# Kernel tuning notes

Hardware: AMD Instinct MI355X
Metric: run time of the kernel (lower is better)

## Reference

```python
import jax, jax.numpy as jnp
import numpy as np

C, P, G = 80, 30000, 800       # classes, preds/class, gts/class
IOU_THR = 0.5
IMG = 1024.0                   # synthetic image size
BATCH = 16                     # images per batch (box[0] = image index)


def _make_boxes(key, n_cls, n):
    """Boxes in the module's 7-col layout: [img_idx, class, score, x1, y1, x2, y2]."""
    k1, k2, k3, k4 = jax.random.split(key, 4)
    xy = jax.random.uniform(k1, (n_cls, n, 2), minval=0.0, maxval=IMG - 128.0)
    wh = jax.random.uniform(k2, (n_cls, n, 2), minval=4.0, maxval=128.0)
    score = jax.random.uniform(k3, (n_cls, n, 1))
    img_idx = jax.random.randint(k4, (n_cls, n, 1), 0, BATCH).astype(jnp.float32)
    cls = jnp.zeros((n_cls, n, 1), jnp.float32)
    return jnp.concatenate([img_idx, cls, score, xy, xy + wh], axis=-1)


def setup_inputs() -> dict:
    key = jax.random.key(0)
    kp, kg = jax.random.split(key)
    return {"pred_boxes": _make_boxes(kp, C, P), "gt_boxes": _make_boxes(kg, C, G)}


def _pairwise_iou(a, b):
    # a: [P,4], b: [G,4] corner-format xyxy -> [P,G]
    lt = jnp.maximum(a[:, None, :2], b[None, :, :2])
    rb = jnp.minimum(a[:, None, 2:], b[None, :, 2:])
    wh = jnp.clip(rb - lt, 0.0)
    inter = wh[..., 0] * wh[..., 1]
    area_a = (a[:, 2] - a[:, 0]) * (a[:, 3] - a[:, 1])
    area_b = (b[:, 2] - b[:, 0]) * (b[:, 3] - b[:, 1])
    return inter / (area_a[:, None] + area_b[None, :] - inter + 1e-9)


def _ap_one_class(pb, gb):
    # pb: [P,7] preds, gb: [G,7] gts for one class
    n_p, n_g = pb.shape[0], gb.shape[0]
    order = jnp.argsort(-pb[:, 2])             # sort preds by score desc
    boxes = pb[order, 3:7]
    iou = _pairwise_iou(boxes, gb[:, 3:7])     # [P,G]
    best_iou = iou.max(axis=1)
    match = iou.argmax(axis=1)                 # best gt per pred
    valid = best_iou > IOU_THR
    p_idx = jnp.arange(n_p, dtype=jnp.int32)
    # first (highest-score) valid pred claiming each gt -> TP; later claims -> FP
    first = jnp.full((n_g,), n_p, jnp.int32).at[match].min(
        jnp.where(valid, p_idx, n_p))
    tp = (valid & (p_idx == first[match])).astype(jnp.float32)
    ctp = jnp.cumsum(tp)
    cfp = jnp.cumsum(1.0 - tp)
    recall = ctp / (n_g + 1e-9)
    precision = ctp / (ctp + cfp + 1e-9)
    # trapezoidal AP over the PR curve (torch.trapz(precisions, recalls))
    return jnp.sum((recall[1:] - recall[:-1]) * (precision[1:] + precision[:-1]) * 0.5)


def reference(pred_boxes, gt_boxes):
    # sequential map over classes keeps peak memory at one [P,G] IoU matrix
    aps = jax.lax.map(lambda ab: _ap_one_class(ab[0], ab[1]), (pred_boxes, gt_boxes))
    return jnp.mean(aps)
```

## Files before the change

### kernel.cpp

```cpp
#include <hip/hip_runtime.h>

#define C 80
#define P 30000
#define G 800
#define BS 256
#define NB 16
#define NC (NB * NB)
#define PPT 8
#define TPB (BS * PPT)


__device__ __forceinline__ unsigned long long pack_key(float s, int p) {
    return ((unsigned long long)__float_as_uint(s) << 32) | (unsigned)(P - 1 - p);
}

__device__ __forceinline__ int cell_of_center(float cxf, float cyf) {
    int bx = min(max((int)(cxf * (1.0f / 64.0f)), 0), NB - 1);
    int by = min(max((int)(cyf * (1.0f / 64.0f)), 0), NB - 1);
    return by * NB + bx;
}

__global__ __launch_bounds__(BS) void gt_bin_kernel(
        const float* __restrict__ gt,
        unsigned short* __restrict__ gtCnt, unsigned short* __restrict__ gtOff,
        float4* __restrict__ gtBox, float* __restrict__ gtAbe,
        unsigned short* __restrict__ gtIdx,
        unsigned long long* __restrict__ gtKey,
        unsigned int* __restrict__ doneCnt) {
    __shared__ int h[NC], cur[NC];
    __shared__ int gcell[G];
    const int c = blockIdx.x, tid = threadIdx.x;
    h[tid] = 0;
    if (c == 0 && tid == 0) *doneCnt = 0u;
    for (int i = tid; i < G; i += BS) gtKey[c * G + i] = 0ull;
    __syncthreads();
    for (int i = tid; i < G; i += BS) {
        const float* r = gt + ((size_t)c * G + i) * 7;
        int cl = cell_of_center(0.5f * (r[3] + r[5]), 0.5f * (r[4] + r[6]));
        gcell[i] = cl;
        atomicAdd(&h[cl], 1);
    }
    __syncthreads();
    const int v = h[tid];
    cur[tid] = v;
    __syncthreads();
    for (int o = 1; o < NC; o <<= 1) {
        int t = (tid >= o) ? cur[tid - o] : 0;
        __syncthreads();
        cur[tid] += t;
        __syncthreads();
    }
    const int excl = cur[tid] - v;
    gtOff[c * NC + tid] = (unsigned short)excl;
    gtCnt[c * NC + tid] = (unsigned short)v;
    __syncthreads();
    cur[tid] = excl;
    __syncthreads();
    for (int i = tid; i < G; i += BS) {
        const float* r = gt + ((size_t)c * G + i) * 7;
        float x1 = r[3], y1 = r[4], x2 = r[5], y2 = r[6];
        int slot = atomicAdd(&cur[gcell[i]], 1);
        gtBox[c * G + slot] = make_float4(x1, y1, x2, y2);
        gtAbe[c * G + slot] = __fadd_rn(__fmul_rn(__fsub_rn(x2, x1), __fsub_rn(y2, y1)), 1e-9f);
        gtIdx[c * G + slot] = (unsigned short)i;
    }
}

__global__ __launch_bounds__(BS) void match7_kernel(
        const float* __restrict__ pred,
        const unsigned short* __restrict__ gtOff, const unsigned short* __restrict__ gtCnt,
        const float4* __restrict__ gtBox, const float* __restrict__ gtAbe,
        const unsigned short* __restrict__ gtIdx,
        unsigned long long* __restrict__ gtKey) {
    __shared__ float4 sB[G];
    __shared__ float  sE[G];
    __shared__ unsigned short sG[G];
    __shared__ unsigned short sOff[NC], sCnt[NC];
    __shared__ unsigned short sIdx[TPB];
    __shared__ int hcnt[NC], bb[NC];
    const int c = blockIdx.y, tid = threadIdx.x;
    const int p0 = blockIdx.x * TPB;
    const int cntP = min(TPB, P - p0);

    for (int i = tid; i < G; i += BS) {
        sB[i] = gtBox[c * G + i];
        sE[i] = gtAbe[c * G + i];
        sG[i] = gtIdx[c * G + i];
    }
    sOff[tid] = gtOff[c * NC + tid];
    sCnt[tid] = gtCnt[c * NC + tid];
    hcnt[tid] = 0;
    __syncthreads();

    const size_t cp = (size_t)c * P;

    unsigned char  cellA[PPT];
    unsigned short lrA[PPT];
    #pragma unroll
    for (int rep = 0; rep < PPT; ++rep) {
        const int li = rep * BS + tid;
        const int p  = p0 + li;
        int cell = 0, lr = 0;
        if (p < P) {
            const float* r = pred + (cp + p) * 7;
            cell = cell_of_center(0.5f * (r[3] + r[5]), 0.5f * (r[4] + r[6]));
            lr = atomicAdd(&hcnt[cell], 1);
        }
        cellA[rep] = (unsigned char)cell;
        lrA[rep] = (unsigned short)lr;
    }
    __syncthreads();

    const int v = hcnt[tid];
    __syncthreads();
    for (int o = 1; o < NC; o <<= 1) {
        int t = (tid >= o) ? hcnt[tid - o] : 0;
        __syncthreads();
        hcnt[tid] += t;
        __syncthreads();
    }
    bb[tid] = hcnt[tid] - v;
    __syncthreads();

    #pragma unroll
    for (int rep = 0; rep < PPT; ++rep) {
        const int li = rep * BS + tid;
        if (p0 + li < P) sIdx[bb[cellA[rep]] + lrA[rep]] = (unsigned short)li;
    }
    __syncthreads();

    #pragma unroll 1
    for (int rep = 0; rep < PPT; ++rep) {
        const int si = rep * BS + tid;
        if (si < cntP) {
            const int li = sIdx[si];
            const int p  = p0 + li;
            const float* r = pred + (cp + p) * 7;
            float ax1 = r[3], ay1 = r[4], ax2 = r[5], ay2 = r[6];
            float A = __fmul_rn(__fsub_rn(ax2, ax1), __fsub_rn(ay2, ay1));
            const int cell = cell_of_center(0.5f * (ax1 + ax2), 0.5f * (ay1 + ay2));
            const int cx = cell & (NB - 1), cy = cell >> 4;
            const int x0 = max(cx - 1, 0), x1 = min(cx + 1, NB - 1);
            const int y0 = max(cy - 1, 0), y1 = min(cy + 1, NB - 1);
            float IN = 0.0f, SB = 1.0f;
            int mj = -1;
            for (int yy = y0; yy <= y1; ++yy) {
                const int rowb = yy * NB;
                const int jb = sOff[rowb + x0];
                const int je = sOff[rowb + x1] + sCnt[rowb + x1];
                #pragma unroll 2
                for (int j = jb; j < je; ++j) {
                    float4 b = sB[j];
                    float lx = fmaxf(ax1, b.x), ly = fmaxf(ay1, b.y);
                    float rx = fminf(ax2, b.z), ry = fminf(ay2, b.w);
                    float wx = fmaxf(__fsub_rn(rx, lx), 0.0f);
                    float wy = fmaxf(__fsub_rn(ry, ly), 0.0f);
                    float in = __fmul_rn(wx, wy);
                    float sb = __fadd_rn(A, sE[j]);
                    bool  up = __fmul_rn(in, SB) > __fmul_rn(IN, sb);
                    IN = up ? in : IN; SB = up ? sb : SB; mj = up ? j : mj;
                }
            }
            if (IN > 0.0f) {
                float4 b = sB[mj];
                float area = __fmul_rn(__fsub_rn(b.z, b.x), __fsub_rn(b.w, b.y));
                float dn = __fadd_rn(__fsub_rn(__fadd_rn(A, area), IN), 1e-9f);
                float iou = __fdiv_rn(IN, dn);
                if (iou > 0.5f) {
                    float sscore = r[2];
                    atomicMax(&gtKey[c * G + sG[mj]], pack_key(sscore, p));
                }
            }
        }
    }
}

__global__ __launch_bounds__(BS) void finale_kernel(
        const float* __restrict__ pred,
        const unsigned long long* __restrict__ gtKey,
        float* __restrict__ ap, unsigned int* __restrict__ doneCnt,
        float* __restrict__ out) {
    __shared__ unsigned long long k[G];
    __shared__ unsigned long long sk[1024];
    __shared__ int h[1024];
    __shared__ int hb[1024];
    __shared__ float red[BS];
    __shared__ int cnt;
    const int c = blockIdx.x, tid = threadIdx.x;

    if (tid == 0) cnt = 0;
    for (int j = tid; j < 1024; j += BS) { sk[j] = 0ull; h[j] = 0; }
    __syncthreads();
    for (int i = tid; i < G; i += BS) {
        unsigned long long key = gtKey[c * G + i];
        if (key != 0ull) k[atomicAdd(&cnt, 1)] = key;
    }
    __syncthreads();
    const int T = cnt;

    for (int t = tid; t < T; t += BS) {
        unsigned long long key = k[t];
        int pos = 0;
        for (int u = 0; u < T; ++u) pos += (k[u] > key) ? 1 : 0;
        sk[pos] = key;
    }
    __syncthreads();

    const float* pr = pred + (size_t)c * P * 7;
    for (int i = tid; i < P; i += BS) {
        unsigned long long kq =
            ((unsigned long long)__float_as_uint(pr[(size_t)i * 7 + 2]) << 32)
            | (unsigned)(P - 1 - i);
        int lo = 0;
        #pragma unroll
        for (int step = 512; step > 0; step >>= 1)
            if (sk[lo + step - 1] > kq) lo += step;
        atomicAdd(&h[lo], 1);
    }
    __syncthreads();

    int* src = h; int* dst = hb;
    for (int o = 1; o < 1024; o <<= 1) {
        for (int j = tid; j < 1024; j += BS)
            dst[j] = src[j] + ((j >= o) ? src[j - o] : 0);
        __syncthreads();
        int* tmp = src; src = dst; dst = tmp;
    }

    float sum = 0.0f;
    for (int s = tid; s < T; s += BS) {
        int r = src[s] - 1;
        if (r >= 1) {
            float kf  = (float)(s + 1);
            float km  = (float)s;
            float ri  = __fdiv_rn(kf, 800.0f);
            float rim = __fdiv_rn(km, 800.0f);
            float pi  = __fdiv_rn(kf, (float)(r + 1));
            float pim = __fdiv_rn(km, (float)r);
            sum = __fadd_rn(sum,
                  __fmul_rn(__fmul_rn(__fsub_rn(ri, rim), __fadd_rn(pi, pim)), 0.5f));
        }
    }
    red[tid] = sum;
    __syncthreads();
    for (int s2 = BS / 2; s2 > 0; s2 >>= 1) {
        if (tid < s2) red[tid] = __fadd_rn(red[tid], red[tid + s2]);
        __syncthreads();
    }
    if (tid == 0) {
        ap[c] = red[0];
        __threadfence();
        unsigned int t = atomicAdd(doneCnt, 1u);
        if (t == C - 1) {
            __threadfence();
            float s = 0.0f;
            for (int c2 = 0; c2 < C; ++c2) s = __fadd_rn(s, ap[c2]);
            out[0] = __fdiv_rn(s, 80.0f);
        }
    }
}

extern "C" void kernel_launch(void* const* d_in, const int* in_sizes, int n_in,
                              void* d_out, int out_size, void* d_ws, size_t ws_size,
                              hipStream_t stream) {
    const float* pred = (const float*)d_in[0];
    const float* gt   = (const float*)d_in[1];
    float* out = (float*)d_out;

    char* ws = (char*)d_ws;
    float*              ap         = (float*)             (ws + 0);
    unsigned int*       doneCnt    = (unsigned int*)      (ws + 512);
    unsigned short*     gtCnt      = (unsigned short*)    (ws + 1024);
    unsigned short*     gtOff      = (unsigned short*)    (ws + 41984);
    unsigned short*     gtIdx      = (unsigned short*)    (ws + 82944);
    float*              gtAbe      = (float*)             (ws + 210944);
    float4*             gtBox      = (float4*)            (ws + 466944);
    unsigned long long* gtKey      = (unsigned long long*)(ws + 1490944);

    const int M_BLK = (P + TPB - 1) / TPB;

    gt_bin_kernel<<<C, BS, 0, stream>>>(gt, gtCnt, gtOff, gtBox, gtAbe, gtIdx,
                                        gtKey, doneCnt);
    match7_kernel<<<dim3(M_BLK, C), BS, 0, stream>>>(pred, gtOff, gtCnt, gtBox,
                                                     gtAbe, gtIdx, gtKey);
    finale_kernel<<<C, BS, 0, stream>>>(pred, gtKey, ap, doneCnt, out);
}
```

Baseline: 280.4 us.

## Split finale into chunked histogram kernel and separate AP scan kernel

The per-class finale kernel, which ran only 80 blocks, is split in two. The first kernel bins all 30000 predictions against the sorted TP keys across 8 chunks per class (640 blocks), merging into a global per-class histogram with atomics. A second small kernel does the prefix scan and the AP sum. This adds parallelism to the binary-search pass, at the cost of one more launch, a global histogram round-trip, and the TP key sort being repeated in every chunk.

```diff
diff --git a/kernel.cpp b/kernel.cpp
--- a/kernel.cpp
+++ b/kernel.cpp
@@ -8,6 +8,8 @@
 #define NC (NB * NB)
 #define PPT 8
 #define TPB (BS * PPT)
+#define HCH 8
+#define CHSZ ((P + HCH - 1) / HCH)
 
 
 __device__ __forceinline__ unsigned long long pack_key(float s, int p) {
@@ -25,7 +27,7 @@
         unsigned short* __restrict__ gtCnt, unsigned short* __restrict__ gtOff,
         float4* __restrict__ gtBox, float* __restrict__ gtAbe,
         unsigned short* __restrict__ gtIdx,
-        unsigned long long* __restrict__ gtKey,
+        unsigned long long* __restrict__ gtKey, int* __restrict__ gHist,
         unsigned int* __restrict__ doneCnt) {
     __shared__ int h[NC], cur[NC];
     __shared__ int gcell[G];
@@ -33,6 +35,7 @@
     h[tid] = 0;
     if (c == 0 && tid == 0) *doneCnt = 0u;
     for (int i = tid; i < G; i += BS) gtKey[c * G + i] = 0ull;
+    for (int j = tid; j < 1024; j += BS) gHist[c * 1024 + j] = 0;
     __syncthreads();
     for (int i = tid; i < G; i += BS) {
         const float* r = gt + ((size_t)c * G + i) * 7;
@@ -175,18 +178,15 @@
     }
 }
 
-__global__ __launch_bounds__(BS) void finale_kernel(
+__global__ __launch_bounds__(BS) void histf_kernel(
         const float* __restrict__ pred,
         const unsigned long long* __restrict__ gtKey,
-        float* __restrict__ ap, unsigned int* __restrict__ doneCnt,
-        float* __restrict__ out) {
+        int* __restrict__ gHist, int* __restrict__ sortT) {
     __shared__ unsigned long long k[G];
     __shared__ unsigned long long sk[1024];
     __shared__ int h[1024];
-    __shared__ int hb[1024];
-    __shared__ float red[BS];
     __shared__ int cnt;
-    const int c = blockIdx.x, tid = threadIdx.x;
+    const int c = blockIdx.y, chunk = blockIdx.x, tid = threadIdx.x;
 
     if (tid == 0) cnt = 0;
     for (int j = tid; j < 1024; j += BS) { sk[j] = 0ull; h[j] = 0; }
@@ -197,6 +197,7 @@
     }
     __syncthreads();
     const int T = cnt;
+    if (chunk == 0 && tid == 0) sortT[c] = T;
 
     for (int t = tid; t < T; t += BS) {
         unsigned long long key = k[t];
@@ -206,8 +207,10 @@
     }
     __syncthreads();
 
+    const int start = chunk * CHSZ;
+    const int end   = min(start + CHSZ, P);
     const float* pr = pred + (size_t)c * P * 7;
-    for (int i = tid; i < P; i += BS) {
+    for (int i = start + tid; i < end; i += BS) {
         unsigned long long kq =
             ((unsigned long long)__float_as_uint(pr[(size_t)i * 7 + 2]) << 32)
             | (unsigned)(P - 1 - i);
@@ -218,15 +221,28 @@
         atomicAdd(&h[lo], 1);
     }
     __syncthreads();
-
-    int* src = h; int* dst = hb;
+    for (int j = tid; j < 1024; j += BS)
+        if (h[j]) atomicAdd(&gHist[c * 1024 + j], h[j]);
+}
+
+__global__ __launch_bounds__(BS) void ap2m_kernel(
+        const int* __restrict__ sortT, const int* __restrict__ gHist,
+        float* __restrict__ ap, unsigned int* __restrict__ doneCnt,
+        float* __restrict__ out) {
+    __shared__ int ha[1024];
+    __shared__ int hb[1024];
+    __shared__ float red[BS];
+    const int c = blockIdx.x, tid = threadIdx.x;
+    const int T = sortT[c];
+    for (int j = tid; j < 1024; j += BS) ha[j] = gHist[c * 1024 + j];
+    __syncthreads();
+    int* src = ha; int* dst = hb;
     for (int o = 1; o < 1024; o <<= 1) {
         for (int j = tid; j < 1024; j += BS)
             dst[j] = src[j] + ((j >= o) ? src[j - o] : 0);
         __syncthreads();
         int* tmp = src; src = dst; dst = tmp;
     }
-
     float sum = 0.0f;
     for (int s = tid; s < T; s += BS) {
         int r = src[s] - 1;
@@ -268,20 +284,23 @@
     float* out = (float*)d_out;
 
     char* ws = (char*)d_ws;
-    float*              ap         = (float*)             (ws + 0);
-    unsigned int*       doneCnt    = (unsigned int*)      (ws + 512);
+    int*                sortT      = (int*)               (ws + 0);
+    float*              ap         = (float*)             (ws + 512);
+    unsigned int*       doneCnt    = (unsigned int*)      (ws + 896);
     unsigned short*     gtCnt      = (unsigned short*)    (ws + 1024);
     unsigned short*     gtOff      = (unsigned short*)    (ws + 41984);
     unsigned short*     gtIdx      = (unsigned short*)    (ws + 82944);
     float*              gtAbe      = (float*)             (ws + 210944);
     float4*             gtBox      = (float4*)            (ws + 466944);
     unsigned long long* gtKey      = (unsigned long long*)(ws + 1490944);
+    int*                gHist      = (int*)               (ws + 2002944);
 
     const int M_BLK = (P + TPB - 1) / TPB;
 
     gt_bin_kernel<<<C, BS, 0, stream>>>(gt, gtCnt, gtOff, gtBox, gtAbe, gtIdx,
-                                        gtKey, doneCnt);
+                                        gtKey, gHist, doneCnt);
     match7_kernel<<<dim3(M_BLK, C), BS, 0, stream>>>(pred, gtOff, gtCnt, gtBox,
                                                      gtAbe, gtIdx, gtKey);
-    finale_kernel<<<C, BS, 0, stream>>>(pred, gtKey, ap, doneCnt, out);
-}
+    histf_kernel<<<dim3(HCH, C), BS, 0, stream>>>(pred, gtKey, gHist, sortT);
+    ap2m_kernel<<<C, BS, 0, stream>>>(sortT, gHist, ap, doneCnt, out);
+}
```

New measurement: 226.7 us. -19.1%, faster.
